# Optimization experiments

Hardware: AMD Instinct MI355X
Metric: run time of the kernel (lower is better)

## Reference

```python
import jax, jax.numpy as jnp
import numpy as np

N = 50000   # nodes
E = 800000  # edges
F = 128     # feat_dim
LN_EPS = 1e-5


def setup_inputs() -> dict:
    key = jax.random.key(0)
    ks = jax.random.split(key, 16)

    def lin(k, fan_in, shape):
        # roughly kaiming-uniform-like scale; exact init is irrelevant for correctness
        return jax.random.normal(k, shape, jnp.float32) * (1.0 / np.sqrt(fan_in))

    inp = {
        "x": jax.random.normal(ks[0], (N, F), jnp.float32),
        "pos": jax.random.normal(ks[1], (N, 3), jnp.float32),
        "edge_index": jax.random.randint(ks[2], (2, E), 0, N, jnp.int64),
        # edge_mlp: Linear(2F+1 -> F), SiLU, Linear(F -> F)
        "ew1": lin(ks[3], 2 * F + 1, (2 * F + 1, F)),
        "eb1": jnp.zeros((F,), jnp.float32),
        "ew2": lin(ks[4], F, (F, F)),
        "eb2": jnp.zeros((F,), jnp.float32),
        # node_mlp: Linear(F -> F), SiLU, Linear(F -> F)
        "nw1": lin(ks[5], F, (F, F)),
        "nb1": jnp.zeros((F,), jnp.float32),
        "nw2": lin(ks[6], F, (F, F)),
        "nb2": jnp.zeros((F,), jnp.float32),
        # coord_mlp: Linear(F -> 1), Tanh
        "cw": lin(ks[7], F, (F, 1)),
        "cb": jnp.zeros((1,), jnp.float32),
        # LayerNorm(F)
        "gamma": jnp.ones((F,), jnp.float32),
        "beta": jnp.zeros((F,), jnp.float32),
    }
    return inp


def reference(x, pos, edge_index, ew1, eb1, ew2, eb2, nw1, nb1, nw2, nb2, cw, cb, gamma, beta):
    row, col = edge_index[0], edge_index[1]

    diff = pos[row] - pos[col]                              # [E, 3]
    dist2 = jnp.sum(diff * diff, axis=1, keepdims=True)     # [E, 1]
    edge_feat = jnp.concatenate([x[row], x[col], dist2], axis=1)  # [E, 2F+1]

    # edge MLP (dropout p=0 -> identity in eval)
    msg = jax.nn.silu(edge_feat @ ew1 + eb1) @ ew2 + eb2    # [E, F]

    # scatter-add messages to source nodes
    agg = jax.ops.segment_sum(msg, row, num_segments=N)     # [N, F]

    # node MLP + residual + LayerNorm
    upd = jax.nn.silu(agg @ nw1 + nb1) @ nw2 + nb2          # [N, F]
    pre = x + upd
    mean = jnp.mean(pre, axis=-1, keepdims=True)
    var = jnp.mean(jnp.square(pre - mean), axis=-1, keepdims=True)
    x_out = gamma * (pre - mean) * jax.lax.rsqrt(var + LN_EPS) + beta

    # coordinate update
    scale = jnp.tanh(msg @ cw + cb)                         # [E, 1]
    delta = jax.ops.segment_sum(scale * diff, row, num_segments=N)  # [N, 3]
    pos_out = pos + delta
    return (x_out, pos_out)
```

## Files before the change

kernel.cpp:

```cpp
#include <hip/hip_runtime.h>
#include <math.h>

#define NN 50000
#define EE 800000
#define FF 128

constexpr float LN_EPS = 1e-5f;
constexpr int NC = (NN + 255) / 256;

typedef float  f32x4  __attribute__((ext_vector_type(4)));
typedef short  s16x8  __attribute__((ext_vector_type(8)));
typedef unsigned short u16x4 __attribute__((ext_vector_type(4)));

__device__ __forceinline__ float silu_f(float v) {
    return v / (1.f + __expf(-v));
}

__device__ __forceinline__ unsigned short f2bf(float f) {
    union { float f; unsigned u; } cv; cv.f = f;
    unsigned u = cv.u;
    u += 0x7fffu + ((u >> 16) & 1u);
    return (unsigned short)(u >> 16);
}

__device__ __forceinline__ float bf2f(unsigned short u) {
    union { unsigned u; float f; } cv; cv.u = ((unsigned)u) << 16;
    return cv.f;
}

constexpr int CVT_BLKS = (NN * FF / 8) / 256;
constexpr int TRW_BLKS = (32768 + 3 * 16384) / 256;

__global__ __launch_bounds__(256) void prep_kernel(
    const float* __restrict__ x, unsigned short* __restrict__ xb,
    const float* __restrict__ ew1, const float* __restrict__ ew2,
    const float* __restrict__ nw1, const float* __restrict__ nw2,
    unsigned short* __restrict__ ew1T, unsigned short* __restrict__ ew2T,
    unsigned short* __restrict__ nw1T, unsigned short* __restrict__ nw2T)
{
    if (blockIdx.x < CVT_BLKS) {
        int i = (blockIdx.x * 256 + threadIdx.x) * 8;
        float4 a = *(const float4*)&x[i];
        float4 b = *(const float4*)&x[i + 4];
        s16x8 o;
        o[0] = (short)f2bf(a.x); o[1] = (short)f2bf(a.y);
        o[2] = (short)f2bf(a.z); o[3] = (short)f2bf(a.w);
        o[4] = (short)f2bf(b.x); o[5] = (short)f2bf(b.y);
        o[6] = (short)f2bf(b.z); o[7] = (short)f2bf(b.w);
        *(s16x8*)&xb[i] = o;
    } else {
        int o = (blockIdx.x - CVT_BLKS) * 256 + threadIdx.x;
        if (o < 32768) {
            int n = o >> 8, k = o & 255;
            ew1T[o] = f2bf(ew1[k * FF + n]);
        } else if (o < 49152) {
            int o2 = o - 32768; int n = o2 >> 7, k = o2 & 127;
            ew2T[o2] = f2bf(ew2[k * FF + n]);
        } else if (o < 65536) {
            int o2 = o - 49152; int n = o2 >> 7, k = o2 & 127;
            nw1T[o2] = f2bf(nw1[k * FF + n]);
        } else {
            int o2 = o - 65536; int n = o2 >> 7, k = o2 & 127;
            nw2T[o2] = f2bf(nw2[k * FF + n]);
        }
    }
}

__global__ __launch_bounds__(256) void hist_kernel(
    const int* __restrict__ ei, int* __restrict__ cnt)
{
    int e = blockIdx.x * 256 + threadIdx.x;
    if (e < EE) atomicAdd(&cnt[ei[e]], 1);
}

__global__ __launch_bounds__(256) void chunk_sum_kernel(
    const int* __restrict__ cnt, int* __restrict__ chunkSum)
{
    __shared__ int s[256];
    int t = threadIdx.x;
    int idx = blockIdx.x * 256 + t;
    s[t] = (idx < NN) ? cnt[idx] : 0;
    __syncthreads();
    for (int off = 128; off > 0; off >>= 1) {
        if (t < off) s[t] += s[t + off];
        __syncthreads();
    }
    if (t == 0) chunkSum[blockIdx.x] = s[0];
}

__global__ __launch_bounds__(256) void scan_chunks_kernel(
    const int* __restrict__ chunkSum, int* __restrict__ chunkOff)
{
    __shared__ int s[256];
    int t = threadIdx.x;
    int v = (t < NC) ? chunkSum[t] : 0;
    s[t] = v;
    __syncthreads();
    for (int off = 1; off < 256; off <<= 1) {
        int u = (t >= off) ? s[t - off] : 0;
        __syncthreads();
        s[t] += u;
        __syncthreads();
    }
    if (t < NC) chunkOff[t] = s[t] - v;
}

__global__ __launch_bounds__(256) void scan_kernel(
    const int* __restrict__ cnt, const int* __restrict__ chunkOff,
    int* __restrict__ offs, int* __restrict__ rowStart)
{
    __shared__ int s[256];
    int t = threadIdx.x;
    int idx = blockIdx.x * 256 + t;
    int v = (idx < NN) ? cnt[idx] : 0;
    s[t] = v;
    __syncthreads();
    for (int off = 1; off < 256; off <<= 1) {
        int u = (t >= off) ? s[t - off] : 0;
        __syncthreads();
        s[t] += u;
        __syncthreads();
    }
    if (idx < NN) {
        int st = chunkOff[blockIdx.x] + s[t] - v;
        offs[idx] = st;
        rowStart[idx] = st;
    }
}

__global__ __launch_bounds__(256) void scatter_idx_kernel(
    const int* __restrict__ ei, int* __restrict__ offs,
    int2* __restrict__ sPair)
{
    int e = blockIdx.x * 256 + threadIdx.x;
    if (e < EE) {
        int r = ei[e], c = ei[EE + e];
        int p = atomicAdd(&offs[r], 1);
        sPair[p] = make_int2(r, c);
    }
}

constexpr int EPB    = 64;
constexpr int NTILE  = EE / EPB;
constexpr int GRID_A = 2500;
constexpr int XAS    = 264;
constexpr int H1S    = 136;
constexpr int MTS    = 72;

__global__ __launch_bounds__(512, 4) void edgeA_kernel(
    const unsigned short* __restrict__ xb, const float* __restrict__ pos,
    const int2* __restrict__ sPair,
    const unsigned short* __restrict__ ew1T, const float* __restrict__ ew1,
    const float* __restrict__ eb1,
    const unsigned short* __restrict__ ew2T, const float* __restrict__ eb2,
    const float* __restrict__ cw,  const float* __restrict__ cb,
    float* __restrict__ agg, float* __restrict__ sSg)
{
    __shared__ float dist2S[EPB];
    __shared__ int   rowS[2][EPB];
    __shared__ float sPartT[EPB][8];
    __shared__ __align__(16) unsigned short xa  [EPB * XAS];
    __shared__ __align__(16) unsigned short h1  [EPB * H1S];
    __shared__ __align__(16) unsigned short msgT[FF * MTS];

    const int t   = threadIdx.x;
    const int w   = t >> 6;
    const int l   = t & 63;
    const int l15 = l & 15;
    const int q8  = l >> 4;
    const int n   = w * 16 + l15;

    int swz;
    {
        const int qd = GRID_A >> 3, r8 = GRID_A & 7;
        int xcd = blockIdx.x & 7, p8 = blockIdx.x >> 3;
        swz = (xcd < r8 ? xcd * (qd + 1) : r8 * (qd + 1) + (xcd - r8) * qd) + p8;
    }

    s16x8 B1[8], B2[4];
    #pragma unroll
    for (int ko = 0; ko < 8; ++ko)
        B1[ko] = *(const s16x8*)(ew1T + (size_t)n * 256 + ko * 32 + q8 * 8);
    #pragma unroll
    for (int ko = 0; ko < 4; ++ko)
        B2[ko] = *(const s16x8*)(ew2T + (size_t)n * 128 + ko * 32 + q8 * 8);
    const float w256 = ew1[256 * FF + n];
    const float b1   = eb1[n];
    const float b2   = eb2[n];
    const float cwc  = cw[n];
    const float cb0  = cb[0];

    const int q    = t & 31;
    const int eB   = t >> 5;
    const int ksel = (q & 15) * 8;
    const bool useRow = (q < 16);

    int   nidx[4];
    s16x8 ag[4];
    {
        int e0 = swz * EPB;
        #pragma unroll
        for (int i = 0; i < 4; ++i) {
            int2 pr = sPair[e0 + eB + 16 * i];
            nidx[i] = useRow ? pr.x : pr.y;
        }
        #pragma unroll
        for (int i = 0; i < 4; ++i) ag[i] = *(const s16x8*)(xb + (size_t)nidx[i] * FF + ksel);
    }

    int bsel = 0;
    for (int tile = swz; tile < NTILE; tile += GRID_A) {
        const int e0 = tile * EPB;

        #pragma unroll
        for (int i = 0; i < 4; ++i)
            *(s16x8*)(xa + (eB + 16 * i) * XAS + q * 8) = ag[i];
        if (t < EPB) {
            int2 pr = sPair[e0 + t];
            int r = pr.x, c = pr.y;
            rowS[bsel][t] = r;
            float dx = pos[r*3+0] - pos[c*3+0];
            float dy = pos[r*3+1] - pos[c*3+1];
            float dz = pos[r*3+2] - pos[c*3+2];
            dist2S[t] = dx*dx + dy*dy + dz*dz;
        }
        __syncthreads();

        {
            int tn  = tile + GRID_A;
            int e0n = (tn < NTILE) ? tn * EPB : 0;
            #pragma unroll
            for (int i = 0; i < 4; ++i) {
                int2 pr = sPair[e0n + eB + 16 * i];
                nidx[i] = useRow ? pr.x : pr.y;
            }
            #pragma unroll
            for (int i = 0; i < 4; ++i) ag[i] = *(const s16x8*)(xb + (size_t)nidx[i] * FF + ksel);
        }

        f32x4 acc[4] = {};
        #pragma unroll
        for (int mt = 0; mt < 4; ++mt) {
            const unsigned short* ar = xa + (mt * 16 + l15) * XAS + q8 * 8;
            #pragma unroll
            for (int ko = 0; ko < 8; ++ko) {
                s16x8 a = *(const s16x8*)(ar + ko * 32);
                acc[mt] = __builtin_amdgcn_mfma_f32_16x16x32_bf16(a, B1[ko], acc[mt], 0, 0, 0);
            }
        }

        #pragma unroll
        for (int mt = 0; mt < 4; ++mt) {
            #pragma unroll
            for (int r = 0; r < 4; ++r) {
                int e = mt * 16 + q8 * 4 + r;
                float v = acc[mt][r] + dist2S[e] * w256 + b1;
                h1[e * H1S + n] = f2bf(silu_f(v));
            }
        }
        __syncthreads();

        f32x4 acc2[4] = {};
        #pragma unroll
        for (int mt = 0; mt < 4; ++mt) {
            const unsigned short* hr = h1 + (mt * 16 + l15) * H1S + q8 * 8;
            #pragma unroll
            for (int ko = 0; ko < 4; ++ko) {
                s16x8 a = *(const s16x8*)(hr + ko * 32);
                acc2[mt] = __builtin_amdgcn_mfma_f32_16x16x32_bf16(a, B2[ko], acc2[mt], 0, 0, 0);
            }
        }

        #pragma unroll
        for (int mt = 0; mt < 4; ++mt) {
            u16x4 o;
            #pragma unroll
            for (int r = 0; r < 4; ++r) {
                float m = acc2[mt][r] + b2;
                o[r] = f2bf(m);
                float p = m * cwc;
                p += __shfl_xor(p, 1);
                p += __shfl_xor(p, 2);
                p += __shfl_xor(p, 4);
                p += __shfl_xor(p, 8);
                if (l15 == 0) sPartT[mt * 16 + q8 * 4 + r][w] = p;
            }
            *(u16x4*)(msgT + n * MTS + mt * 16 + q8 * 4) = o;
        }
        __syncthreads();

        {
            int e  = t >> 3;
            int ww = t & 7;
            float p = sPartT[e][ww];
            p += __shfl_xor(p, 1);
            p += __shfl_xor(p, 2);
            p += __shfl_xor(p, 4);
            if (ww == 0) sSg[e0 + e] = tanhf(p + cb0);
        }

        {
            int c    = t & 127;
            int s    = t >> 7;
            int base = s * 16;
            const unsigned short* mr = msgT + c * MTS + base;
            s16x8 v0 = *(const s16x8*)(mr);
            s16x8 v1 = *(const s16x8*)(mr + 8);
            float a  = 0.f;
            int cur  = rowS[bsel][base];
            #pragma unroll
            for (int k = 0; k < 16; ++k) {
                int r = rowS[bsel][base + k];
                if (r != cur) {
                    atomicAdd(&agg[(size_t)cur * FF + c], a);
                    a = 0.f; cur = r;
                }
                unsigned short mv = (k < 8) ? (unsigned short)v0[k]
                                            : (unsigned short)v1[k - 8];
                a += bf2f(mv);
            }
            atomicAdd(&agg[(size_t)cur * FF + c], a);
        }
        bsel ^= 1;
    }
}

constexpr int NPB  = 64;
constexpr int ABS  = 136;
constexpr int NBLK = (NN + NPB - 1) / NPB;

__global__ __launch_bounds__(512) void nodeB_kernel(
    const float* __restrict__ x, const float* __restrict__ pos,
    const float* __restrict__ agg, const float* __restrict__ sSg,
    const int2* __restrict__ sPair, const int* __restrict__ rowStart,
    const unsigned short* __restrict__ nw1T, const float* __restrict__ nb1,
    const unsigned short* __restrict__ nw2T, const float* __restrict__ nb2,
    const float* __restrict__ gamma, const float* __restrict__ beta,
    float* __restrict__ xout, float* __restrict__ posout)
{
    __shared__ __align__(16) unsigned short aB [NPB * ABS];
    __shared__ __align__(16) unsigned short h1B[NPB * ABS];
    __shared__ float sRedS[8][NPB];
    __shared__ float sRedQ[8][NPB];

    const int t   = threadIdx.x;
    const int w   = t >> 6;
    const int l   = t & 63;
    const int l15 = l & 15;
    const int q8  = l >> 4;
    const int n0  = blockIdx.x * NPB;
    const int n   = w * 16 + l15;

    #pragma unroll
    for (int i = 0; i < 4; ++i) {
        int idx = (i * 512 + t) * 4;
        int e = idx >> 7, c = idx & 127;
        u16x4 o;
        if (n0 + e < NN) {
            float4 v = *(const float4*)&agg[(size_t)(n0 + e) * FF + c];
            o[0] = f2bf(v.x); o[1] = f2bf(v.y); o[2] = f2bf(v.z); o[3] = f2bf(v.w);
        } else {
            o[0] = 0; o[1] = 0; o[2] = 0; o[3] = 0;
        }
        *(u16x4*)(aB + e * ABS + c) = o;
    }

    {
        int e  = t >> 3;
        int ch = t & 7;
        int nn = n0 + e;
        bool ok = nn < NN;
        int p0 = ok ? rowStart[nn] : 0;
        int p1 = ok ? ((nn == NN - 1) ? EE : rowStart[nn + 1]) : 0;
        float px = ok ? pos[nn*3+0] : 0.f;
        float py = ok ? pos[nn*3+1] : 0.f;
        float pz = ok ? pos[nn*3+2] : 0.f;
        float sx = 0.f, sy = 0.f, sz = 0.f;
        for (int p = p0 + ch; p < p1; p += 8) {
            int c = sPair[p].y;
            float g = sSg[p];
            sx += g * (px - pos[c*3+0]);
            sy += g * (py - pos[c*3+1]);
            sz += g * (pz - pos[c*3+2]);
        }
        #pragma unroll
        for (int off = 1; off < 8; off <<= 1) {
            sx += __shfl_xor(sx, off);
            sy += __shfl_xor(sy, off);
            sz += __shfl_xor(sz, off);
        }
        if (ch == 0 && ok) {
            posout[nn*3+0] = px + sx;
            posout[nn*3+1] = py + sy;
            posout[nn*3+2] = pz + sz;
        }
    }
    __syncthreads();

    f32x4 acc[4] = {};
    {
        s16x8 bw[4];
        #pragma unroll
        for (int ko = 0; ko < 4; ++ko)
            bw[ko] = *(const s16x8*)(nw1T + (size_t)n * 128 + ko * 32 + q8 * 8);
        #pragma unroll
        for (int mt = 0; mt < 4; ++mt) {
            const unsigned short* ar = aB + (mt * 16 + l15) * ABS + q8 * 8;
            #pragma unroll
            for (int ko = 0; ko < 4; ++ko) {
                s16x8 a = *(const s16x8*)(ar + ko * 32);
                acc[mt] = __builtin_amdgcn_mfma_f32_16x16x32_bf16(a, bw[ko], acc[mt], 0, 0, 0);
            }
        }
    }
    {
        float bb = nb1[n];
        #pragma unroll
        for (int mt = 0; mt < 4; ++mt) {
            #pragma unroll
            for (int r = 0; r < 4; ++r) {
                int e = mt * 16 + q8 * 4 + r;
                h1B[e * ABS + n] = f2bf(silu_f(acc[mt][r] + bb));
            }
        }
    }
    __syncthreads();

    f32x4 acc2[4] = {};
    {
        s16x8 bw[4];
        #pragma unroll
        for (int ko = 0; ko < 4; ++ko)
            bw[ko] = *(const s16x8*)(nw2T + (size_t)n * 128 + ko * 32 + q8 * 8);
        #pragma unroll
        for (int mt = 0; mt < 4; ++mt) {
            const unsigned short* hr = h1B + (mt * 16 + l15) * ABS + q8 * 8;
            #pragma unroll
            for (int ko = 0; ko < 4; ++ko) {
                s16x8 a = *(const s16x8*)(hr + ko * 32);
                acc2[mt] = __builtin_amdgcn_mfma_f32_16x16x32_bf16(a, bw[ko], acc2[mt], 0, 0, 0);
            }
        }
    }

    float pre[4][4];
    {
        float bb = nb2[n];
        #pragma unroll
        for (int mt = 0; mt < 4; ++mt) {
            #pragma unroll
            for (int r = 0; r < 4; ++r) {
                int e  = mt * 16 + q8 * 4 + r;
                int nn = n0 + e;
                float xv = (nn < NN) ? x[(size_t)nn * FF + n] : 0.f;
                pre[mt][r] = xv + acc2[mt][r] + bb;
            }
        }
    }
    #pragma unroll
    for (int mt = 0; mt < 4; ++mt) {
        #pragma unroll
        for (int r = 0; r < 4; ++r) {
            float s = pre[mt][r], sq = pre[mt][r] * pre[mt][r];
            s += __shfl_xor(s, 1);  sq += __shfl_xor(sq, 1);
            s += __shfl_xor(s, 2);  sq += __shfl_xor(sq, 2);
            s += __shfl_xor(s, 4);  sq += __shfl_xor(sq, 4);
            s += __shfl_xor(s, 8);  sq += __shfl_xor(sq, 8);
            if (l15 == 0) {
                int e = mt * 16 + q8 * 4 + r;
                sRedS[w][e] = s;
                sRedQ[w][e] = sq;
            }
        }
    }
    __syncthreads();

    {
        float g = gamma[n], bt = beta[n];
        #pragma unroll
        for (int mt = 0; mt < 4; ++mt) {
            #pragma unroll
            for (int r = 0; r < 4; ++r) {
                int e  = mt * 16 + q8 * 4 + r;
                int nn = n0 + e;
                if (nn < NN) {
                    float S = 0.f, Q = 0.f;
                    #pragma unroll
                    for (int ww = 0; ww < 8; ++ww) { S += sRedS[ww][e]; Q += sRedQ[ww][e]; }
                    float mean = S * (1.f / FF);
                    float var  = Q * (1.f / FF) - mean * mean;
                    xout[(size_t)nn * FF + n] =
                        g * (pre[mt][r] - mean) * rsqrtf(var + LN_EPS) + bt;
                }
            }
        }
    }
}

extern "C" void kernel_launch(void* const* d_in, const int* in_sizes, int n_in,
                              void* d_out, int out_size, void* d_ws, size_t ws_size,
                              hipStream_t stream) {
    const float* x    = (const float*)d_in[0];
    const float* pos  = (const float*)d_in[1];
    const int*   ei   = (const int*)  d_in[2];
    const float* ew1  = (const float*)d_in[3];
    const float* eb1  = (const float*)d_in[4];
    const float* ew2  = (const float*)d_in[5];
    const float* eb2  = (const float*)d_in[6];
    const float* nw1  = (const float*)d_in[7];
    const float* nb1  = (const float*)d_in[8];
    const float* nw2  = (const float*)d_in[9];
    const float* nb2  = (const float*)d_in[10];
    const float* cw   = (const float*)d_in[11];
    const float* cb   = (const float*)d_in[12];
    const float* gam  = (const float*)d_in[13];
    const float* bet  = (const float*)d_in[14];

    float* out    = (float*)d_out;
    float* xout   = out;
    float* posout = out + (size_t)NN * FF;

    auto align256 = [](size_t v) { return (v + 255) & ~(size_t)255; };
    char* ws = (char*)d_ws;

    size_t CNT_B   = align256((size_t)NN * 4);
    size_t OFFS_B  = align256((size_t)NN * 4);
    size_t RST_B   = align256((size_t)NN * 4);
    size_t CHNK_B  = align256((size_t)NC * 4 * 2);
    size_t SPAIR_B = align256((size_t)EE * 8);
    size_t XB_B    = align256((size_t)NN * FF * 2);
    size_t EW1T_B  = align256((size_t)128 * 256 * 2);
    size_t WT_B    = align256((size_t)128 * 128 * 2);
    size_t AGG_B   = align256((size_t)NN * FF * 4);

    size_t o = 0;
    int* cnt       = (int*)(ws + o);  o += CNT_B;
    int* offs      = (int*)(ws + o);  o += OFFS_B;
    int* rowStart  = (int*)(ws + o);  o += RST_B;
    int* chunkSum  = (int*)(ws + o);
    int* chunkOff  = chunkSum + NC;   o += CHNK_B;
    int2* sPair    = (int2*)(ws + o); o += SPAIR_B;
    unsigned short* xb   = (unsigned short*)(ws + o);  o += XB_B;
    unsigned short* ew1T = (unsigned short*)(ws + o);  o += EW1T_B;
    unsigned short* ew2T = (unsigned short*)(ws + o);  o += WT_B;
    unsigned short* nw1T = (unsigned short*)(ws + o);  o += WT_B;
    unsigned short* nw2T = (unsigned short*)(ws + o);  o += WT_B;
    float*          agg  = (float*)(ws + o);           o += AGG_B;
    float*          sSg  = (float*)(ws + o);

    hipMemsetAsync(cnt, 0, CNT_B, stream);
    hipMemsetAsync(agg, 0, (size_t)NN * FF * 4, stream);

    prep_kernel<<<CVT_BLKS + TRW_BLKS, 256, 0, stream>>>(
        x, xb, ew1, ew2, nw1, nw2, ew1T, ew2T, nw1T, nw2T);

    hist_kernel<<<(EE + 255) / 256, 256, 0, stream>>>(ei, cnt);
    chunk_sum_kernel<<<NC, 256, 0, stream>>>(cnt, chunkSum);
    scan_chunks_kernel<<<1, 256, 0, stream>>>(chunkSum, chunkOff);
    scan_kernel<<<NC, 256, 0, stream>>>(cnt, chunkOff, offs, rowStart);
    scatter_idx_kernel<<<(EE + 255) / 256, 256, 0, stream>>>(ei, offs, sPair);

    edgeA_kernel<<<GRID_A, 512, 0, stream>>>(
        xb, pos, sPair, ew1T, ew1, eb1, ew2T, eb2, cw, cb, agg, sSg);

    nodeB_kernel<<<NBLK, 512, 0, stream>>>(
        x, pos, agg, sSg, sPair, rowStart,
        nw1T, nb1, nw2T, nb2, gam, bet, xout, posout);
}
```

Baseline: 494.9 us.

## Precompute per-node first-layer projections and gather them per edge

Splits the first edge-MLP layer into per-node products x@W_row and x@W_col, computed once per node in a new MFMA kernel and stored as bf16. The edge kernel then gathers these projected rows, adds them with the dist2 term and bias, and applies SiLU, dropping the 256-wide GEMM per edge. This cuts edge-side matrix work at the cost of an extra node kernel, a 50000x256 bf16 buffer, and an extra bf16 rounding of the partial sums.

```diff
diff --git a/kernel.cpp b/kernel.cpp
--- a/kernel.cpp
+++ b/kernel.cpp
@@ -66,6 +66,65 @@
     }
 }
 
+constexpr int YABS = 136;
+constexpr int YNBLK = (NN + 63) / 64;
+
+__global__ __launch_bounds__(512) void nodeY_kernel(
+    const unsigned short* __restrict__ xb,
+    const unsigned short* __restrict__ ew1T,
+    unsigned short* __restrict__ Y)
+{
+    __shared__ __align__(16) unsigned short aB[64 * YABS];
+
+    const int t   = threadIdx.x;
+    const int w   = t >> 6;
+    const int l   = t & 63;
+    const int l15 = l & 15;
+    const int q8  = l >> 4;
+    const int n0  = blockIdx.x * 64;
+    const int n   = w * 16 + l15;
+
+    #pragma unroll
+    for (int i = 0; i < 2; ++i) {
+        int idx = (i * 512 + t) * 8;
+        int e = idx >> 7, c = idx & 127;
+        s16x8 v = {};
+        if (n0 + e < NN) v = *(const s16x8*)(xb + (size_t)(n0 + e) * FF + c);
+        *(s16x8*)(aB + e * YABS + c) = v;
+    }
+    __syncthreads();
+
+    s16x8 ba[4], bb[4];
+    #pragma unroll
+    for (int ko = 0; ko < 4; ++ko) {
+        ba[ko] = *(const s16x8*)(ew1T + (size_t)n * 256 + ko * 32 + q8 * 8);
+        bb[ko] = *(const s16x8*)(ew1T + (size_t)n * 256 + 128 + ko * 32 + q8 * 8);
+    }
+
+    f32x4 acc1[4] = {}, acc2[4] = {};
+    #pragma unroll
+    for (int mt = 0; mt < 4; ++mt) {
+        const unsigned short* ar = aB + (mt * 16 + l15) * YABS + q8 * 8;
+        #pragma unroll
+        for (int ko = 0; ko < 4; ++ko) {
+            s16x8 a = *(const s16x8*)(ar + ko * 32);
+            acc1[mt] = __builtin_amdgcn_mfma_f32_16x16x32_bf16(a, ba[ko], acc1[mt], 0, 0, 0);
+            acc2[mt] = __builtin_amdgcn_mfma_f32_16x16x32_bf16(a, bb[ko], acc2[mt], 0, 0, 0);
+        }
+    }
+    #pragma unroll
+    for (int mt = 0; mt < 4; ++mt) {
+        #pragma unroll
+        for (int r = 0; r < 4; ++r) {
+            int nn = n0 + mt * 16 + q8 * 4 + r;
+            if (nn < NN) {
+                Y[(size_t)nn * 256 + n]       = f2bf(acc1[mt][r]);
+                Y[(size_t)nn * 256 + 128 + n] = f2bf(acc2[mt][r]);
+            }
+        }
+    }
+}
+
 __global__ __launch_bounds__(256) void hist_kernel(
     const int* __restrict__ ei, int* __restrict__ cnt)
 {
@@ -148,10 +207,9 @@
 constexpr int MTS    = 72;
 
 __global__ __launch_bounds__(512, 4) void edgeA_kernel(
-    const unsigned short* __restrict__ xb, const float* __restrict__ pos,
+    const unsigned short* __restrict__ Yb, const float* __restrict__ pos,
     const int2* __restrict__ sPair,
-    const unsigned short* __restrict__ ew1T, const float* __restrict__ ew1,
-    const float* __restrict__ eb1,
+    const float* __restrict__ ew1, const float* __restrict__ eb1,
     const unsigned short* __restrict__ ew2T, const float* __restrict__ eb2,
     const float* __restrict__ cw,  const float* __restrict__ cb,
     float* __restrict__ agg, float* __restrict__ sSg)
@@ -159,7 +217,7 @@
     __shared__ float dist2S[EPB];
     __shared__ int   rowS[2][EPB];
     __shared__ float sPartT[EPB][8];
-    __shared__ __align__(16) unsigned short xa  [EPB * XAS];
+    __shared__ __align__(16) unsigned short ya  [EPB * XAS];
     __shared__ __align__(16) unsigned short h1  [EPB * H1S];
     __shared__ __align__(16) unsigned short msgT[FF * MTS];
 
@@ -177,23 +235,33 @@
         swz = (xcd < r8 ? xcd * (qd + 1) : r8 * (qd + 1) + (xcd - r8) * qd) + p8;
     }
 
-    s16x8 B1[8], B2[4];
-    #pragma unroll
-    for (int ko = 0; ko < 8; ++ko)
-        B1[ko] = *(const s16x8*)(ew1T + (size_t)n * 256 + ko * 32 + q8 * 8);
+    s16x8 B2[4];
     #pragma unroll
     for (int ko = 0; ko < 4; ++ko)
         B2[ko] = *(const s16x8*)(ew2T + (size_t)n * 128 + ko * 32 + q8 * 8);
-    const float w256 = ew1[256 * FF + n];
-    const float b1   = eb1[n];
     const float b2   = eb2[n];
     const float cwc  = cw[n];
     const float cb0  = cb[0];
+
+    const int c8 = (t & 15) * 8;
+    const int e2 = (t >> 4) * 2;
+    float w256r[8], b1r[8];
+    {
+        float4 wa = *(const float4*)&ew1[256 * FF + c8];
+        float4 wb = *(const float4*)&ew1[256 * FF + c8 + 4];
+        w256r[0]=wa.x; w256r[1]=wa.y; w256r[2]=wa.z; w256r[3]=wa.w;
+        w256r[4]=wb.x; w256r[5]=wb.y; w256r[6]=wb.z; w256r[7]=wb.w;
+        float4 ca = *(const float4*)&eb1[c8];
+        float4 cbv = *(const float4*)&eb1[c8 + 4];
+        b1r[0]=ca.x; b1r[1]=ca.y; b1r[2]=ca.z; b1r[3]=ca.w;
+        b1r[4]=cbv.x; b1r[5]=cbv.y; b1r[6]=cbv.z; b1r[7]=cbv.w;
+    }
 
     const int q    = t & 31;
     const int eB   = t >> 5;
     const int ksel = (q & 15) * 8;
     const bool useRow = (q < 16);
+    const int colOff = useRow ? 0 : 128;
 
     int   nidx[4];
     s16x8 ag[4];
@@ -205,7 +273,8 @@
             nidx[i] = useRow ? pr.x : pr.y;
         }
         #pragma unroll
-        for (int i = 0; i < 4; ++i) ag[i] = *(const s16x8*)(xb + (size_t)nidx[i] * FF + ksel);
+        for (int i = 0; i < 4; ++i)
+            ag[i] = *(const s16x8*)(Yb + (size_t)nidx[i] * 256 + colOff + ksel);
     }
 
     int bsel = 0;
@@ -214,7 +283,7 @@
 
         #pragma unroll
         for (int i = 0; i < 4; ++i)
-            *(s16x8*)(xa + (eB + 16 * i) * XAS + q * 8) = ag[i];
+            *(s16x8*)(ya + (eB + 16 * i) * XAS + q * 8) = ag[i];
         if (t < EPB) {
             int2 pr = sPair[e0 + t];
             int r = pr.x, c = pr.y;
@@ -235,28 +304,24 @@
                 nidx[i] = useRow ? pr.x : pr.y;
             }
             #pragma unroll
-            for (int i = 0; i < 4; ++i) ag[i] = *(const s16x8*)(xb + (size_t)nidx[i] * FF + ksel);
-        }
-
-        f32x4 acc[4] = {};
-        #pragma unroll
-        for (int mt = 0; mt < 4; ++mt) {
-            const unsigned short* ar = xa + (mt * 16 + l15) * XAS + q8 * 8;
-            #pragma unroll
-            for (int ko = 0; ko < 8; ++ko) {
-                s16x8 a = *(const s16x8*)(ar + ko * 32);
-                acc[mt] = __builtin_amdgcn_mfma_f32_16x16x32_bf16(a, B1[ko], acc[mt], 0, 0, 0);
-            }
-        }
-
-        #pragma unroll
-        for (int mt = 0; mt < 4; ++mt) {
-            #pragma unroll
-            for (int r = 0; r < 4; ++r) {
-                int e = mt * 16 + q8 * 4 + r;
-                float v = acc[mt][r] + dist2S[e] * w256 + b1;
-                h1[e * H1S + n] = f2bf(silu_f(v));
-            }
+            for (int i = 0; i < 4; ++i)
+                ag[i] = *(const s16x8*)(Yb + (size_t)nidx[i] * 256 + colOff + ksel);
+        }
+
+        #pragma unroll
+        for (int s = 0; s < 2; ++s) {
+            int e = e2 + s;
+            s16x8 y1 = *(const s16x8*)(ya + e * XAS + c8);
+            s16x8 y2 = *(const s16x8*)(ya + e * XAS + 128 + c8);
+            float d2 = dist2S[e];
+            s16x8 o;
+            #pragma unroll
+            for (int j = 0; j < 8; ++j) {
+                float v = bf2f((unsigned short)y1[j]) + bf2f((unsigned short)y2[j])
+                        + d2 * w256r[j] + b1r[j];
+                o[j] = (short)f2bf(silu_f(v));
+            }
+            *(s16x8*)(h1 + e * H1S + c8) = o;
         }
         __syncthreads();
 
@@ -531,6 +596,7 @@
     size_t XB_B    = align256((size_t)NN * FF * 2);
     size_t EW1T_B  = align256((size_t)128 * 256 * 2);
     size_t WT_B    = align256((size_t)128 * 128 * 2);
+    size_t Y_B     = align256((size_t)NN * 256 * 2);
     size_t AGG_B   = align256((size_t)NN * FF * 4);
 
     size_t o = 0;
@@ -545,6 +611,7 @@
     unsigned short* ew2T = (unsigned short*)(ws + o);  o += WT_B;
     unsigned short* nw1T = (unsigned short*)(ws + o);  o += WT_B;
     unsigned short* nw2T = (unsigned short*)(ws + o);  o += WT_B;
+    unsigned short* Yb   = (unsigned short*)(ws + o);  o += Y_B;
     float*          agg  = (float*)(ws + o);           o += AGG_B;
     float*          sSg  = (float*)(ws + o);
 
@@ -553,6 +620,8 @@
 
     prep_kernel<<<CVT_BLKS + TRW_BLKS, 256, 0, stream>>>(
         x, xb, ew1, ew2, nw1, nw2, ew1T, ew2T, nw1T, nw2T);
+
+    nodeY_kernel<<<YNBLK, 512, 0, stream>>>(xb, ew1T, Yb);
 
     hist_kernel<<<(EE + 255) / 256, 256, 0, stream>>>(ei, cnt);
     chunk_sum_kernel<<<NC, 256, 0, stream>>>(cnt, chunkSum);
@@ -561,7 +630,7 @@
     scatter_idx_kernel<<<(EE + 255) / 256, 256, 0, stream>>>(ei, offs, sPair);
 
     edgeA_kernel<<<GRID_A, 512, 0, stream>>>(
-        xb, pos, sPair, ew1T, ew1, eb1, ew2T, eb2, cw, cb, agg, sSg);
+        Yb, pos, sPair, ew1, eb1, ew2T, eb2, cw, cb, agg, sSg);
 
     nodeB_kernel<<<NBLK, 512, 0, stream>>>(
         x, pos, agg, sSg, sPair, rowStart,
```

After: 465.6 us. 1.06x faster.
